# Performance work log

Hardware: AMD Instinct MI355X
Metric: run time of the kernel (lower is better)

The kernel has to match this reference:

```python
import jax, jax.numpy as jnp
import numpy as np

N = 50000
E = 250000
NUM_ETYPES = 4
H = 2  # num_heads
EPS = 1e-12


def _gat_conv(x, W, al, ar, b, src, dst):
    # x: (N, in_dim); W: (in_dim, H*D); al/ar/b: (H, D); src/dst: (E,)
    D = al.shape[-1]
    feat = (x @ W).reshape(-1, H, D)            # (N, H, D)
    el = jnp.sum(feat * al, axis=-1)            # (N, H)
    er = jnp.sum(feat * ar, axis=-1)            # (N, H)
    e = jax.nn.leaky_relu(el[src] + er[dst], 0.2)   # (E, H)
    emax = jax.ops.segment_max(e, dst, num_segments=N)
    ex = jnp.exp(e - emax[dst])
    denom = jax.ops.segment_sum(ex, dst, num_segments=N)
    alpha = ex / denom[dst]                     # (E, H) segment softmax over in-edges
    msg = feat[src] * alpha[:, :, None]         # (E, H, D)
    out = jax.ops.segment_sum(msg, dst, num_segments=N)  # (N, H, D)
    return out + b


def _hetero_layer(x, W, al, ar, b, edges):
    # vmap GATConv over the edge-type axis, then HeteroGraphConv aggregate='mean'
    outs = jax.vmap(lambda w, a, r, bb, e: _gat_conv(x, w, a, r, bb, e[0], e[1]))(
        W, al, ar, b, edges)                    # (T, N, H, D)
    return jnp.mean(outs, axis=0)               # (N, H, D)


def _post(v):
    # relu -> F.normalize(dim=1, i.e. across heads) -> dropout(eval: identity) -> mean over heads
    v = jax.nn.relu(v)
    norm = jnp.sqrt(jnp.sum(v * v, axis=1, keepdims=True))
    v = v / jnp.maximum(norm, EPS)
    return jnp.mean(v, axis=1)                  # (N, D)


def setup_inputs() -> dict:
    key = jax.random.key(0)
    ks = jax.random.split(key, 16)
    s = 0.05
    inp = {
        'x': jax.random.normal(ks[0], (N, 23), jnp.float32),
        'edges': jax.random.randint(ks[1], (NUM_ETYPES, 2, E), 0, N, jnp.int32),
        'W0': jax.random.normal(ks[2], (NUM_ETYPES, 23, H * 64), jnp.float32) * s,
        'al0': jax.random.normal(ks[3], (NUM_ETYPES, H, 64), jnp.float32) * s,
        'ar0': jax.random.normal(ks[4], (NUM_ETYPES, H, 64), jnp.float32) * s,
        'b0': jnp.zeros((NUM_ETYPES, H, 64), jnp.float32),
        'W1': jax.random.normal(ks[5], (NUM_ETYPES, 64, H * 64), jnp.float32) * s,
        'al1': jax.random.normal(ks[6], (NUM_ETYPES, H, 64), jnp.float32) * s,
        'ar1': jax.random.normal(ks[7], (NUM_ETYPES, H, 64), jnp.float32) * s,
        'b1': jnp.zeros((NUM_ETYPES, H, 64), jnp.float32),
        'W2': jax.random.normal(ks[8], (NUM_ETYPES, 64, H * 64), jnp.float32) * s,
        'al2': jax.random.normal(ks[9], (NUM_ETYPES, H, 64), jnp.float32) * s,
        'ar2': jax.random.normal(ks[10], (NUM_ETYPES, H, 64), jnp.float32) * s,
        'b2': jnp.zeros((NUM_ETYPES, H, 64), jnp.float32),
    }
    return inp


def reference(x, edges, W0, al0, ar0, b0, W1, al1, ar1, b1, W2, al2, ar2, b2):
    h = x  # feature_by_level, feat_level=0
    h = _post(_hetero_layer(h, W0, al0, ar0, b0, edges))
    h = _post(_hetero_layer(h, W1, al1, ar1, b1, edges))
    h = jnp.mean(_hetero_layer(h, W2, al2, ar2, b2, edges), axis=1)  # (N, out_dim)
    out = jnp.mean(h, axis=0, keepdims=True)    # dgl.mean_nodes, single graph -> (1, out_dim)
    return out
```

## Files before the change

kernel.cpp:

```cpp
#include <hip/hip_runtime.h>

#define NN 50000
#define NE 250000
#define SCAN_LEN (4*NN)
#define SCAN_BLKS ((SCAN_LEN + 255)/256)
#define EDGE_BLKS ((4*NE + 255)/256)

typedef __attribute__((ext_vector_type(8))) short bf16x8;
typedef __attribute__((ext_vector_type(4))) float f32x4;

__device__ inline ushort f2bf(float f) {
  uint u = __float_as_uint(f);
  return (ushort)((u + 0x7fffu + ((u >> 16) & 1u)) >> 16);
}
__device__ inline float bf2f(ushort b) { return __uint_as_float(((uint)b) << 16); }

__global__ __launch_bounds__(256) void zero_ints(int* __restrict__ p, int n) {
  int i = blockIdx.x*256 + threadIdx.x;
  if (i < n) p[i] = 0;
}
__global__ __launch_bounds__(256) void zero_floats(float* __restrict__ p, int n) {
  int i = blockIdx.x*256 + threadIdx.x;
  if (i < n) p[i] = 0.f;
}

__global__ __launch_bounds__(256) void count_kernel(const int* __restrict__ edges, int* __restrict__ counts) {
  int idx = blockIdx.x*256 + threadIdx.x;
  if (idx >= 4*NE) return;
  int t = idx / NE, e = idx - t*NE;
  int dst = edges[(size_t)t*2*NE + NE + e];
  atomicAdd(&counts[t*NN + dst], 1);
}

__global__ __launch_bounds__(256) void scan1_kernel(const int* __restrict__ in, int* __restrict__ out, int* __restrict__ bsum) {
  __shared__ int sd[256];
  int i = blockIdx.x*256 + threadIdx.x;
  int v = (i < SCAN_LEN) ? in[i] : 0;
  sd[threadIdx.x] = v;
  __syncthreads();
  for (int off = 1; off < 256; off <<= 1) {
    int add = (threadIdx.x >= off) ? sd[threadIdx.x - off] : 0;
    __syncthreads();
    sd[threadIdx.x] += add;
    __syncthreads();
  }
  if (i < SCAN_LEN) out[i] = sd[threadIdx.x] - v;
  if (threadIdx.x == 255) bsum[blockIdx.x] = sd[255];
}

__global__ __launch_bounds__(1024) void scan2_kernel(int* __restrict__ bsum, int nb) {
  __shared__ int sd[1024];
  int i = threadIdx.x;
  int v = (i < nb) ? bsum[i] : 0;
  sd[i] = v;
  __syncthreads();
  for (int off = 1; off < 1024; off <<= 1) {
    int add = (i >= off) ? sd[i - off] : 0;
    __syncthreads();
    sd[i] += add;
    __syncthreads();
  }
  if (i < nb) bsum[i] = sd[i] - v;
}

__global__ __launch_bounds__(256) void scan3_kernel(int* __restrict__ row_ptr, const int* __restrict__ bsum, int* __restrict__ cursor) {
  int i = blockIdx.x*256 + threadIdx.x;
  if (i < SCAN_LEN) {
    int val = row_ptr[i] + bsum[blockIdx.x];
    row_ptr[i] = val;
    cursor[i] = val;
  }
  if (i == 0) row_ptr[SCAN_LEN] = 4*NE;
}

__global__ __launch_bounds__(256) void scatter_kernel(const int* __restrict__ edges, int* __restrict__ cursor, int* __restrict__ col_idx) {
  int idx = blockIdx.x*256 + threadIdx.x;
  if (idx >= 4*NE) return;
  int t = idx / NE, e = idx - t*NE;
  int src = edges[(size_t)t*2*NE + e];
  int dst = edges[(size_t)t*2*NE + NE + e];
  int pos = atomicAdd(&cursor[t*NN + dst], 1);
  col_idx[pos] = src;
}

__global__ __launch_bounds__(256) void convert_x_kernel(const float* __restrict__ x, ushort* __restrict__ xpad) {
  int i = blockIdx.x*256 + threadIdx.x;
  if (i >= NN*64) return;
  int k = i & 63, n = i >> 6;
  xpad[i] = (k < 23) ? f2bf(x[n*23 + k]) : (ushort)0;
}
__global__ __launch_bounds__(256) void convert_wt_kernel(const float* __restrict__ W, ushort* __restrict__ WTg, int Kin) {
  int i = blockIdx.x*256 + threadIdx.x;
  if (i >= 4*128*64) return;
  int k = i & 63, c = (i >> 6) & 127, t = i >> 13;
  float w = (k < Kin) ? W[((size_t)t*Kin + k)*128 + c] : 0.f;
  WTg[i] = f2bf(w);
}

__global__ __launch_bounds__(256)
void gemm_mfma_kernel(const ushort* __restrict__ hbf,
                      const ushort* __restrict__ WTg,
                      const float* __restrict__ alall, const float* __restrict__ arall,
                      ushort* __restrict__ feat, float* __restrict__ el, float* __restrict__ er)
{
  __shared__ ushort WT[128*64];
  const int t = blockIdx.y;
  const int tid = threadIdx.x;
  const int wv = tid >> 6, lane = tid & 63;
  const int node0 = blockIdx.x*64;

  {
    const ushort* src = WTg + (size_t)t*128*64;
    #pragma unroll
    for (int q = 0; q < 4; ++q) {
      int cc = tid + q*256;
      int c = cc >> 3, jj = cc & 7;
      bf16x8 val = *(const bf16x8*)(src + cc*8);
      *(bf16x8*)((char*)WT + c*128 + ((jj ^ (c & 7))*16)) = val;
    }
  }
  __syncthreads();

  const int mrow = lane & 15;
  const int kq = lane >> 4;
  const int anode = node0 + wv*16 + mrow;

  const bf16x8 a0 = *(const bf16x8*)(hbf + (size_t)anode*64 + kq*8);
  const bf16x8 a1 = *(const bf16x8*)(hbf + (size_t)anode*64 + 32 + kq*8);

  f32x4 acc[8];
  #pragma unroll
  for (int nb = 0; nb < 8; ++nb) acc[nb] = (f32x4){0.f,0.f,0.f,0.f};

  #pragma unroll
  for (int nb = 0; nb < 8; ++nb) {
    const int c = nb*16 + mrow;
    const bf16x8 b0 = *(const bf16x8*)((const char*)WT + c*128 + ((kq       ^ (c&7))*16));
    const bf16x8 b1 = *(const bf16x8*)((const char*)WT + c*128 + (((4 + kq) ^ (c&7))*16));
    acc[nb] = __builtin_amdgcn_mfma_f32_16x16x32_bf16(a0, b0, acc[nb], 0, 0, 0);
    acc[nb] = __builtin_amdgcn_mfma_f32_16x16x32_bf16(a1, b1, acc[nb], 0, 0, 0);
  }

  float elp[4][2] = {{0,0},{0,0},{0,0},{0,0}};
  float erp[4][2] = {{0,0},{0,0},{0,0},{0,0}};
  const int noder = node0 + wv*16 + kq*4;
  #pragma unroll
  for (int nb = 0; nb < 8; ++nb) {
    const int c = nb*16 + mrow;
    const float alv = alall[t*128 + c];
    const float arv = arall[t*128 + c];
    const int head = nb >> 2;
    #pragma unroll
    for (int r = 0; r < 4; ++r) {
      elp[r][head] += acc[nb][r]*alv;
      erp[r][head] += acc[nb][r]*arv;
      if (noder + r < NN)
        feat[((size_t)t*NN + noder + r)*128 + c] = f2bf(acc[nb][r]);
    }
  }
  #pragma unroll
  for (int off = 1; off < 16; off <<= 1) {
    #pragma unroll
    for (int r = 0; r < 4; ++r) {
      elp[r][0] += __shfl_xor(elp[r][0], off); elp[r][1] += __shfl_xor(elp[r][1], off);
      erp[r][0] += __shfl_xor(erp[r][0], off); erp[r][1] += __shfl_xor(erp[r][1], off);
    }
  }
  if (mrow == 0) {
    #pragma unroll
    for (int r = 0; r < 4; ++r) {
      if (noder + r < NN) {
        const size_t ix = ((size_t)t*NN + noder + r)*2;
        el[ix]   = elp[r][0]; el[ix+1] = elp[r][1];
        er[ix]   = erp[r][0]; er[ix+1] = erp[r][1];
      }
    }
  }
}

__global__ __launch_bounds__(256)
void gat_node_kernel(const ushort* __restrict__ feat, const float* __restrict__ el,
                     const float* __restrict__ er, const int* __restrict__ row_ptr,
                     const int* __restrict__ col_idx, const float* __restrict__ ball,
                     ushort* __restrict__ hout, int post)
{
  const int v = __builtin_amdgcn_readfirstlane(blockIdx.x*4 + (threadIdx.x >> 6));
  const int lane = threadIdx.x & 63;
  const int half = lane >> 5;
  const int j = lane & 31;

  float ax = 0.f, ay = 0.f;

  for (int t = 0; t < 4; ++t) {
    const int rp0 = row_ptr[t*NN + v];
    const int deg = row_ptr[t*NN + v + 1] - rp0;
    if (deg <= 0) continue;
    const float* elt = el + (size_t)t*NN*2;
    const uint* ftu = (const uint*)(feat + (size_t)t*NN*128);
    const float2 epair = *(const float2*)&er[((size_t)t*NN + v)*2];
    const float erv = half ? epair.y : epair.x;

    float s_run = 0.f, tx = 0.f, ty = 0.f;
    for (int base = 0; base < deg; base += 32) {
      const int cnt = min(32, deg - base);
      int s = 0; float p = 0.f;
      if (j < cnt) {
        s = col_idx[rp0 + base + j];
        float u = elt[s*2 + half] + erv;
        u = (u > 0.f) ? u : 0.2f*u;
        p = __expf(fminf(fmaxf(u, -60.f), 60.f));
      }
      float ps = p;
      #pragma unroll
      for (int off = 16; off; off >>= 1) ps += __shfl_xor(ps, off);
      s_run += ps;

      const uint pbits = __float_as_uint(p);
      const int cnt4 = (cnt + 3) & ~3;
      for (int q0 = 0; q0 < cnt4; q0 += 4) {
        #pragma unroll
        for (int u4 = 0; u4 < 4; ++u4) {
          const int q = q0 + u4;
          const int   sq  = __builtin_amdgcn_readlane(s, q);
          const float pq0 = __uint_as_float(__builtin_amdgcn_readlane(pbits, q));
          const float pq1 = __uint_as_float(__builtin_amdgcn_readlane(pbits, 32 + q));
          const float pq  = half ? pq1 : pq0;
          const uint w = ftu[(uint)sq*64u + (uint)lane];
          tx += pq * __uint_as_float(w << 16);
          ty += pq * __uint_as_float(w & 0xffff0000u);
        }
      }
    }
    const float inv = 1.f / s_run;
    ax += tx*inv; ay += ty*inv;
  }

  const int d0 = lane*2;
  float bx = 0.f, by = 0.f;
  #pragma unroll
  for (int t = 0; t < 4; ++t) { bx += ball[t*128 + d0]; by += ball[t*128 + d0 + 1]; }
  ax = 0.25f*(ax + bx); ay = 0.25f*(ay + by);

  if (post) { ax = fmaxf(ax, 0.f); ay = fmaxf(ay, 0.f); }
  const float px = __shfl_xor(ax, 32), py = __shfl_xor(ay, 32);
  if (lane < 32) {
    float ox, oy;
    if (post) {
      ox = 0.5f*(ax + px)/fmaxf(sqrtf(ax*ax + px*px), 1e-12f);
      oy = 0.5f*(ay + py)/fmaxf(sqrtf(ay*ay + py*py), 1e-12f);
    } else {
      ox = 0.5f*(ax + px); oy = 0.5f*(ay + py);
    }
    const uint pk = (uint)f2bf(ox) | ((uint)f2bf(oy) << 16);
    *(uint*)(hout + (size_t)v*64 + d0) = pk;
  }
}

__global__ __launch_bounds__(256) void reduce_nodes(const ushort* __restrict__ hn, float* __restrict__ accum) {
  __shared__ float sd[256];
  int d = threadIdx.x & 63, rg = threadIdx.x >> 6;
  float s = 0.f;
  for (int r = blockIdx.x*4 + rg; r < NN; r += gridDim.x*4) s += bf2f(hn[(size_t)r*64 + d]);
  sd[threadIdx.x] = s;
  __syncthreads();
  if (threadIdx.x < 64) {
    s = sd[threadIdx.x] + sd[threadIdx.x+64] + sd[threadIdx.x+128] + sd[threadIdx.x+192];
    atomicAdd(&accum[threadIdx.x], s);
  }
}
__global__ __launch_bounds__(64) void final_out_kernel(const float* __restrict__ accum, float* __restrict__ out) {
  int d = threadIdx.x;
  if (d < 64) out[d] = accum[d] * (1.0f/NN);
}

extern "C" void kernel_launch(void* const* d_in, const int* in_sizes, int n_in,
                              void* d_out, int out_size, void* d_ws, size_t ws_size,
                              hipStream_t stream) {
  const float* x     = (const float*)d_in[0];
  const int*   edges = (const int*)d_in[1];
  const float* W[3]  = {(const float*)d_in[2], (const float*)d_in[6], (const float*)d_in[10]};
  const float* al[3] = {(const float*)d_in[3], (const float*)d_in[7], (const float*)d_in[11]};
  const float* ar[3] = {(const float*)d_in[4], (const float*)d_in[8], (const float*)d_in[12]};
  const float* b[3]  = {(const float*)d_in[5], (const float*)d_in[9], (const float*)d_in[13]};

  char* ws = (char*)d_ws;
  auto up = [](size_t x_) { return (x_ + 255) & ~(size_t)255; };

  const size_t szFeat = (size_t)4*NN*128*sizeof(ushort);
  const size_t szEl   = (size_t)4*NN*2*sizeof(float);
  const size_t szHB   = (size_t)(NN+64)*64*sizeof(ushort);
  const size_t szWT   = (size_t)4*128*64*sizeof(ushort);
  const size_t szRp   = (size_t)(4*NN+1)*sizeof(int);
  const size_t szCnt  = (size_t)4*NN*sizeof(int);
  const size_t szCi   = (size_t)4*NE*sizeof(int);

  size_t o = 0;
  ushort* feat  = (ushort*)(ws + o); o += up(szFeat);
  float* elbuf  = (float*)(ws + o);  o += up(szEl);
  float* erbuf  = (float*)(ws + o);  o += up(szEl);
  ushort* xpad  = (ushort*)(ws + o); o += up(szHB);
  ushort* hbuf  = (ushort*)(ws + o); o += up(szHB);
  ushort* WTg   = (ushort*)(ws + o); o += up(szWT);
  float* accum  = (float*)(ws + o);  o += up(256);
  int* row_ptr  = (int*)(ws + o);    o += up(szRp);
  int* cursor   = (int*)(ws + o);    o += up(szCnt);
  int* counts   = (int*)(ws + o);    o += up(szCnt);
  int* col_idx  = (int*)(ws + o);    o += up(szCi);
  int* bsum     = (int*)(ws + o);    o += up(4096);

  zero_ints<<<(4*NN + 255)/256, 256, 0, stream>>>(counts, 4*NN);
  count_kernel<<<EDGE_BLKS, 256, 0, stream>>>(edges, counts);
  scan1_kernel<<<SCAN_BLKS, 256, 0, stream>>>(counts, row_ptr, bsum);
  scan2_kernel<<<1, 1024, 0, stream>>>(bsum, SCAN_BLKS);
  scan3_kernel<<<SCAN_BLKS, 256, 0, stream>>>(row_ptr, bsum, cursor);
  scatter_kernel<<<EDGE_BLKS, 256, 0, stream>>>(edges, cursor, col_idx);

  convert_x_kernel<<<(NN*64 + 255)/256, 256, 0, stream>>>(x, xpad);

  const int gemmGX = (NN + 63)/64;

  for (int l = 0; l < 3; ++l) {
    const ushort* hin = (l == 0) ? xpad : hbuf;
    convert_wt_kernel<<<(4*128*64 + 255)/256, 256, 0, stream>>>(W[l], WTg, (l == 0) ? 23 : 64);
    gemm_mfma_kernel<<<dim3(gemmGX, 4), 256, 0, stream>>>(hin, WTg, al[l], ar[l], feat, elbuf, erbuf);
    gat_node_kernel<<<NN/4, 256, 0, stream>>>(feat, elbuf, erbuf, row_ptr, col_idx, b[l], hbuf, (l < 2) ? 1 : 0);
  }

  zero_floats<<<1, 64, 0, stream>>>(accum, 64);
  reduce_nodes<<<256, 256, 0, stream>>>(hbuf, accum);
  final_out_kernel<<<1, 64, 0, stream>>>(accum, (float*)d_out);
}
```

Baseline: 410.5 us.

## Merge per-type CSR into per-node CSR, precompute edge softmax weights, fold attention into GEMM

Builds one CSR keyed by destination node, with per-type sub-ranges and source indices offset by type, so the gather kernel walks all four edge types for a node in one contiguous range. Attention logits el/er are folded into the GEMM as four extra weight columns (W·a precomputed). A separate edge-parallel kernel computes the exp weights, and the gather kernel becomes a simple per-edge loop without readlane broadcasts. Features are stored with head-interleaved packing so each lane handles one dimension for both heads. The cost is an extra edge pass per layer plus posmap/pexp buffers. Logits are now rounded to bf16 through the MFMA path, which lowers precision.

```diff
diff --git a/kernel.cpp b/kernel.cpp
--- a/kernel.cpp
+++ b/kernel.cpp
@@ -2,8 +2,7 @@
 
 #define NN 50000
 #define NE 250000
-#define SCAN_LEN (4*NN)
-#define SCAN_BLKS ((SCAN_LEN + 255)/256)
+#define NSCAN_BLKS ((NN + 255)/256)
 #define EDGE_BLKS ((4*NE + 255)/256)
 
 typedef __attribute__((ext_vector_type(8))) short bf16x8;
@@ -32,10 +31,15 @@
   atomicAdd(&counts[t*NN + dst], 1);
 }
 
-__global__ __launch_bounds__(256) void scan1_kernel(const int* __restrict__ in, int* __restrict__ out, int* __restrict__ bsum) {
+__global__ __launch_bounds__(256) void sumdeg_kernel(const int* __restrict__ counts, int* __restrict__ totdeg) {
+  int v = blockIdx.x*256 + threadIdx.x;
+  if (v < NN) totdeg[v] = counts[v] + counts[NN+v] + counts[2*NN+v] + counts[3*NN+v];
+}
+
+__global__ __launch_bounds__(256) void scan1_kernel(const int* __restrict__ in, int* __restrict__ out, int* __restrict__ bsum, int n) {
   __shared__ int sd[256];
   int i = blockIdx.x*256 + threadIdx.x;
-  int v = (i < SCAN_LEN) ? in[i] : 0;
+  int v = (i < n) ? in[i] : 0;
   sd[threadIdx.x] = v;
   __syncthreads();
   for (int off = 1; off < 256; off <<= 1) {
@@ -44,7 +48,7 @@
     sd[threadIdx.x] += add;
     __syncthreads();
   }
-  if (i < SCAN_LEN) out[i] = sd[threadIdx.x] - v;
+  if (i < n) out[i] = sd[threadIdx.x] - v;
   if (threadIdx.x == 255) bsum[blockIdx.x] = sd[255];
 }
 
@@ -63,24 +67,34 @@
   if (i < nb) bsum[i] = sd[i] - v;
 }
 
-__global__ __launch_bounds__(256) void scan3_kernel(int* __restrict__ row_ptr, const int* __restrict__ bsum, int* __restrict__ cursor) {
-  int i = blockIdx.x*256 + threadIdx.x;
-  if (i < SCAN_LEN) {
-    int val = row_ptr[i] + bsum[blockIdx.x];
-    row_ptr[i] = val;
-    cursor[i] = val;
-  }
-  if (i == 0) row_ptr[SCAN_LEN] = 4*NE;
-}
-
-__global__ __launch_bounds__(256) void scatter_kernel(const int* __restrict__ edges, int* __restrict__ cursor, int* __restrict__ col_idx) {
+__global__ __launch_bounds__(256) void scan3b_kernel(int* __restrict__ rp, const int* __restrict__ bsum, int n, int total) {
+  int i = blockIdx.x*256 + threadIdx.x;
+  if (i < n) rp[i] += bsum[blockIdx.x];
+  if (i == 0) rp[n] = total;
+}
+
+__global__ __launch_bounds__(256) void make_cursor_kernel(const int* __restrict__ rp2, const int* __restrict__ counts,
+                                                          int* __restrict__ cursor, int* __restrict__ sub_ptr) {
+  int v = blockIdx.x*256 + threadIdx.x;
+  if (v >= NN) return;
+  int b = rp2[v];
+  int s1 = b  + counts[v];
+  int s2 = s1 + counts[NN+v];
+  int s3 = s2 + counts[2*NN+v];
+  cursor[v] = b; cursor[NN+v] = s1; cursor[2*NN+v] = s2; cursor[3*NN+v] = s3;
+  sub_ptr[NN+v] = s1; sub_ptr[2*NN+v] = s2; sub_ptr[3*NN+v] = s3;
+}
+
+__global__ __launch_bounds__(256) void scatter2_kernel(const int* __restrict__ edges, int* __restrict__ cursor,
+                                                       int* __restrict__ col2, int* __restrict__ posmap) {
   int idx = blockIdx.x*256 + threadIdx.x;
   if (idx >= 4*NE) return;
   int t = idx / NE, e = idx - t*NE;
   int src = edges[(size_t)t*2*NE + e];
   int dst = edges[(size_t)t*2*NE + NE + e];
   int pos = atomicAdd(&cursor[t*NN + dst], 1);
-  col_idx[pos] = src;
+  col2[pos] = t*NN + src;
+  posmap[idx] = pos;
 }
 
 __global__ __launch_bounds__(256) void convert_x_kernel(const float* __restrict__ x, ushort* __restrict__ xpad) {
@@ -89,33 +103,43 @@
   int k = i & 63, n = i >> 6;
   xpad[i] = (k < 23) ? f2bf(x[n*23 + k]) : (ushort)0;
 }
-__global__ __launch_bounds__(256) void convert_wt_kernel(const float* __restrict__ W, ushort* __restrict__ WTg, int Kin) {
-  int i = blockIdx.x*256 + threadIdx.x;
-  if (i >= 4*128*64) return;
-  int k = i & 63, c = (i >> 6) & 127, t = i >> 13;
-  float w = (k < Kin) ? W[((size_t)t*Kin + k)*128 + c] : 0.f;
-  WTg[i] = f2bf(w);
+
+__global__ __launch_bounds__(256) void convert_wt2_kernel(const float* __restrict__ W, const float* __restrict__ al,
+                                                          const float* __restrict__ ar, ushort* __restrict__ WTg2, int Kin) {
+  int i = blockIdx.x*256 + threadIdx.x;
+  if (i >= 4*144*64) return;
+  int k = i & 63; int c = (i >> 6) % 144; int t = i / (144*64);
+  float val = 0.f;
+  if (c < 128) {
+    val = (k < Kin) ? W[((size_t)t*Kin + k)*128 + c] : 0.f;
+  } else if (c < 132 && k < Kin) {
+    int m = c - 128, h = m & 1;
+    const float* A = ((m < 2) ? al : ar) + t*128 + h*64;
+    const float* wrow = W + ((size_t)t*Kin + k)*128 + h*64;
+    float s = 0.f;
+    for (int c2 = 0; c2 < 64; ++c2) s += wrow[c2]*A[c2];
+    val = s;
+  }
+  WTg2[((size_t)t*144 + c)*64 + k] = f2bf(val);
 }
 
 __global__ __launch_bounds__(256)
 void gemm_mfma_kernel(const ushort* __restrict__ hbf,
-                      const ushort* __restrict__ WTg,
-                      const float* __restrict__ alall, const float* __restrict__ arall,
-                      ushort* __restrict__ feat, float* __restrict__ el, float* __restrict__ er)
+                      const ushort* __restrict__ WTg2,
+                      uint* __restrict__ featu,
+                      float* __restrict__ elr)
 {
-  __shared__ ushort WT[128*64];
+  __shared__ ushort WT[144*64];
   const int t = blockIdx.y;
   const int tid = threadIdx.x;
   const int wv = tid >> 6, lane = tid & 63;
   const int node0 = blockIdx.x*64;
 
   {
-    const ushort* src = WTg + (size_t)t*128*64;
-    #pragma unroll
-    for (int q = 0; q < 4; ++q) {
-      int cc = tid + q*256;
-      int c = cc >> 3, jj = cc & 7;
-      bf16x8 val = *(const bf16x8*)(src + cc*8);
+    const ushort* src = WTg2 + (size_t)t*144*64;
+    for (int i = tid; i < 1152; i += 256) {
+      int c = i >> 3, jj = i & 7;
+      bf16x8 val = *(const bf16x8*)(src + (size_t)c*64 + jj*8);
       *(bf16x8*)((char*)WT + c*128 + ((jj ^ (c & 7))*16)) = val;
     }
   }
@@ -128,12 +152,12 @@
   const bf16x8 a0 = *(const bf16x8*)(hbf + (size_t)anode*64 + kq*8);
   const bf16x8 a1 = *(const bf16x8*)(hbf + (size_t)anode*64 + 32 + kq*8);
 
-  f32x4 acc[8];
-  #pragma unroll
-  for (int nb = 0; nb < 8; ++nb) acc[nb] = (f32x4){0.f,0.f,0.f,0.f};
-
-  #pragma unroll
-  for (int nb = 0; nb < 8; ++nb) {
+  f32x4 acc[9];
+  #pragma unroll
+  for (int nb = 0; nb < 9; ++nb) acc[nb] = (f32x4){0.f,0.f,0.f,0.f};
+
+  #pragma unroll
+  for (int nb = 0; nb < 9; ++nb) {
     const int c = nb*16 + mrow;
     const bf16x8 b0 = *(const bf16x8*)((const char*)WT + c*128 + ((kq       ^ (c&7))*16));
     const bf16x8 b1 = *(const bf16x8*)((const char*)WT + c*128 + (((4 + kq) ^ (c&7))*16));
@@ -141,119 +165,93 @@
     acc[nb] = __builtin_amdgcn_mfma_f32_16x16x32_bf16(a1, b1, acc[nb], 0, 0, 0);
   }
 
-  float elp[4][2] = {{0,0},{0,0},{0,0},{0,0}};
-  float erp[4][2] = {{0,0},{0,0},{0,0},{0,0}};
   const int noder = node0 + wv*16 + kq*4;
   #pragma unroll
-  for (int nb = 0; nb < 8; ++nb) {
-    const int c = nb*16 + mrow;
-    const float alv = alall[t*128 + c];
-    const float arv = arall[t*128 + c];
-    const int head = nb >> 2;
-    #pragma unroll
-    for (int r = 0; r < 4; ++r) {
-      elp[r][head] += acc[nb][r]*alv;
-      erp[r][head] += acc[nb][r]*arv;
-      if (noder + r < NN)
-        feat[((size_t)t*NN + noder + r)*128 + c] = f2bf(acc[nb][r]);
-    }
-  }
-  #pragma unroll
-  for (int off = 1; off < 16; off <<= 1) {
-    #pragma unroll
-    for (int r = 0; r < 4; ++r) {
-      elp[r][0] += __shfl_xor(elp[r][0], off); elp[r][1] += __shfl_xor(elp[r][1], off);
-      erp[r][0] += __shfl_xor(erp[r][0], off); erp[r][1] += __shfl_xor(erp[r][1], off);
-    }
-  }
-  if (mrow == 0) {
+  for (int nb = 0; nb < 4; ++nb) {
+    const int d = nb*16 + mrow;
     #pragma unroll
     for (int r = 0; r < 4; ++r) {
       if (noder + r < NN) {
-        const size_t ix = ((size_t)t*NN + noder + r)*2;
-        el[ix]   = elp[r][0]; el[ix+1] = elp[r][1];
-        er[ix]   = erp[r][0]; er[ix+1] = erp[r][1];
+        const uint pk = (uint)f2bf(acc[nb][r]) | ((uint)f2bf(acc[nb+4][r]) << 16);
+        featu[((size_t)t*NN + noder + r)*64 + d] = pk;
       }
     }
   }
+  if (mrow < 4) {
+    #pragma unroll
+    for (int r = 0; r < 4; ++r) {
+      if (noder + r < NN)
+        elr[(size_t)(mrow*4 + t)*NN + noder + r] = acc[8][r];
+    }
+  }
 }
 
 __global__ __launch_bounds__(256)
-void gat_node_kernel(const ushort* __restrict__ feat, const float* __restrict__ el,
-                     const float* __restrict__ er, const int* __restrict__ row_ptr,
-                     const int* __restrict__ col_idx, const float* __restrict__ ball,
-                     ushort* __restrict__ hout, int post)
+void phaseA_kernel(const int* __restrict__ edges, const float* __restrict__ elr,
+                   const int* __restrict__ posmap, float* __restrict__ pexp)
+{
+  int idx = blockIdx.x*256 + threadIdx.x;
+  if (idx >= 4*NE) return;
+  int t = idx / NE, e = idx - t*NE;
+  int src = edges[(size_t)t*2*NE + e];
+  int dst = edges[(size_t)t*2*NE + NE + e];
+  float u0 = elr[(size_t)(0*4+t)*NN + src] + elr[(size_t)(2*4+t)*NN + dst];
+  float u1 = elr[(size_t)(1*4+t)*NN + src] + elr[(size_t)(3*4+t)*NN + dst];
+  u0 = (u0 > 0.f) ? u0 : 0.2f*u0;
+  u1 = (u1 > 0.f) ? u1 : 0.2f*u1;
+  float p0 = __expf(fminf(fmaxf(u0, -60.f), 60.f));
+  float p1 = __expf(fminf(fmaxf(u1, -60.f), 60.f));
+  int pos = posmap[idx];
+  ((float2*)pexp)[pos] = make_float2(p0, p1);
+}
+
+__global__ __launch_bounds__(256)
+void gather_kernel(const uint* __restrict__ featu, const float* __restrict__ pexp,
+                   const int* __restrict__ col2, const int* __restrict__ row_ptr2,
+                   const int* __restrict__ sub_ptr, const float* __restrict__ ball,
+                   ushort* __restrict__ hout, int post)
 {
   const int v = __builtin_amdgcn_readfirstlane(blockIdx.x*4 + (threadIdx.x >> 6));
   const int lane = threadIdx.x & 63;
-  const int half = lane >> 5;
-  const int j = lane & 31;
+
+  const int b0 = row_ptr2[v];
+  const int b4 = row_ptr2[v+1];
+  const int s1 = sub_ptr[NN+v], s2 = sub_ptr[2*NN+v], s3 = sub_ptr[3*NN+v];
+  const int bounds[5] = {b0, s1, s2, s3, b4};
 
   float ax = 0.f, ay = 0.f;
 
+  #pragma unroll
   for (int t = 0; t < 4; ++t) {
-    const int rp0 = row_ptr[t*NN + v];
-    const int deg = row_ptr[t*NN + v + 1] - rp0;
-    if (deg <= 0) continue;
-    const float* elt = el + (size_t)t*NN*2;
-    const uint* ftu = (const uint*)(feat + (size_t)t*NN*128);
-    const float2 epair = *(const float2*)&er[((size_t)t*NN + v)*2];
-    const float erv = half ? epair.y : epair.x;
-
-    float s_run = 0.f, tx = 0.f, ty = 0.f;
-    for (int base = 0; base < deg; base += 32) {
-      const int cnt = min(32, deg - base);
-      int s = 0; float p = 0.f;
-      if (j < cnt) {
-        s = col_idx[rp0 + base + j];
-        float u = elt[s*2 + half] + erv;
-        u = (u > 0.f) ? u : 0.2f*u;
-        p = __expf(fminf(fmaxf(u, -60.f), 60.f));
-      }
-      float ps = p;
-      #pragma unroll
-      for (int off = 16; off; off >>= 1) ps += __shfl_xor(ps, off);
-      s_run += ps;
-
-      const uint pbits = __float_as_uint(p);
-      const int cnt4 = (cnt + 3) & ~3;
-      for (int q0 = 0; q0 < cnt4; q0 += 4) {
-        #pragma unroll
-        for (int u4 = 0; u4 < 4; ++u4) {
-          const int q = q0 + u4;
-          const int   sq  = __builtin_amdgcn_readlane(s, q);
-          const float pq0 = __uint_as_float(__builtin_amdgcn_readlane(pbits, q));
-          const float pq1 = __uint_as_float(__builtin_amdgcn_readlane(pbits, 32 + q));
-          const float pq  = half ? pq1 : pq0;
-          const uint w = ftu[(uint)sq*64u + (uint)lane];
-          tx += pq * __uint_as_float(w << 16);
-          ty += pq * __uint_as_float(w & 0xffff0000u);
-        }
-      }
+    const int lo = bounds[t], hi = bounds[t+1];
+    if (lo >= hi) continue;
+    float sum0 = 0.f, sum1 = 0.f, tx = 0.f, ty = 0.f;
+    #pragma unroll 4
+    for (int q = lo; q < hi; ++q) {
+      const int c = col2[q];
+      const float2 p = ((const float2*)pexp)[q];
+      sum0 += p.x; sum1 += p.y;
+      const uint w = featu[(uint)c*64u + (uint)lane];
+      tx += p.x * __uint_as_float(w << 16);
+      ty += p.y * __uint_as_float(w & 0xffff0000u);
     }
-    const float inv = 1.f / s_run;
-    ax += tx*inv; ay += ty*inv;
-  }
-
-  const int d0 = lane*2;
+    ax += tx * __builtin_amdgcn_rcpf(sum0);
+    ay += ty * __builtin_amdgcn_rcpf(sum1);
+  }
+
   float bx = 0.f, by = 0.f;
   #pragma unroll
-  for (int t = 0; t < 4; ++t) { bx += ball[t*128 + d0]; by += ball[t*128 + d0 + 1]; }
+  for (int t = 0; t < 4; ++t) { bx += ball[t*128 + lane]; by += ball[t*128 + 64 + lane]; }
   ax = 0.25f*(ax + bx); ay = 0.25f*(ay + by);
 
-  if (post) { ax = fmaxf(ax, 0.f); ay = fmaxf(ay, 0.f); }
-  const float px = __shfl_xor(ax, 32), py = __shfl_xor(ay, 32);
-  if (lane < 32) {
-    float ox, oy;
-    if (post) {
-      ox = 0.5f*(ax + px)/fmaxf(sqrtf(ax*ax + px*px), 1e-12f);
-      oy = 0.5f*(ay + py)/fmaxf(sqrtf(ay*ay + py*py), 1e-12f);
-    } else {
-      ox = 0.5f*(ax + px); oy = 0.5f*(ay + py);
-    }
-    const uint pk = (uint)f2bf(ox) | ((uint)f2bf(oy) << 16);
-    *(uint*)(hout + (size_t)v*64 + d0) = pk;
-  }
+  float o;
+  if (post) {
+    ax = fmaxf(ax, 0.f); ay = fmaxf(ay, 0.f);
+    o = 0.5f*(ax + ay) / fmaxf(sqrtf(ax*ax + ay*ay), 1e-12f);
+  } else {
+    o = 0.5f*(ax + ay);
+  }
+  hout[(size_t)v*64 + lane] = f2bf(o);
 }
 
 __global__ __launch_bounds__(256) void reduce_nodes(const ushort* __restrict__ hn, float* __restrict__ accum) {
@@ -286,34 +284,40 @@
   char* ws = (char*)d_ws;
   auto up = [](size_t x_) { return (x_ + 255) & ~(size_t)255; };
 
-  const size_t szFeat = (size_t)4*NN*128*sizeof(ushort);
-  const size_t szEl   = (size_t)4*NN*2*sizeof(float);
+  const size_t szFeat = (size_t)4*NN*64*sizeof(uint);
+  const size_t szElr  = (size_t)16*NN*sizeof(float);
+  const size_t szPex  = (size_t)4*NE*2*sizeof(float);
+  const size_t szPM   = (size_t)4*NE*sizeof(int);
   const size_t szHB   = (size_t)(NN+64)*64*sizeof(ushort);
-  const size_t szWT   = (size_t)4*128*64*sizeof(ushort);
-  const size_t szRp   = (size_t)(4*NN+1)*sizeof(int);
-  const size_t szCnt  = (size_t)4*NN*sizeof(int);
-  const size_t szCi   = (size_t)4*NE*sizeof(int);
+  const size_t szWT   = (size_t)4*144*64*sizeof(ushort);
+  const size_t szI4   = (size_t)4*NN*sizeof(int);
+  const size_t szI1   = (size_t)(NN+1)*sizeof(int);
 
   size_t o = 0;
-  ushort* feat  = (ushort*)(ws + o); o += up(szFeat);
-  float* elbuf  = (float*)(ws + o);  o += up(szEl);
-  float* erbuf  = (float*)(ws + o);  o += up(szEl);
-  ushort* xpad  = (ushort*)(ws + o); o += up(szHB);
-  ushort* hbuf  = (ushort*)(ws + o); o += up(szHB);
-  ushort* WTg   = (ushort*)(ws + o); o += up(szWT);
-  float* accum  = (float*)(ws + o);  o += up(256);
-  int* row_ptr  = (int*)(ws + o);    o += up(szRp);
-  int* cursor   = (int*)(ws + o);    o += up(szCnt);
-  int* counts   = (int*)(ws + o);    o += up(szCnt);
-  int* col_idx  = (int*)(ws + o);    o += up(szCi);
-  int* bsum     = (int*)(ws + o);    o += up(4096);
+  uint*   featu  = (uint*)(ws + o);   o += up(szFeat);
+  float*  elr    = (float*)(ws + o);  o += up(szElr);
+  float*  pexp   = (float*)(ws + o);  o += up(szPex);
+  int*    posmap = (int*)(ws + o);    o += up(szPM);
+  int*    col2   = (int*)(ws + o);    o += up(szPM);
+  ushort* xpad   = (ushort*)(ws + o); o += up(szHB);
+  ushort* hbuf   = (ushort*)(ws + o); o += up(szHB);
+  ushort* WTg2   = (ushort*)(ws + o); o += up(szWT);
+  float*  accum  = (float*)(ws + o);  o += up(256);
+  int* row_ptr2  = (int*)(ws + o);    o += up(szI1);
+  int* totdeg    = (int*)(ws + o);    o += up(szI1);
+  int* cursor    = (int*)(ws + o);    o += up(szI4);
+  int* counts    = (int*)(ws + o);    o += up(szI4);
+  int* sub_ptr   = (int*)(ws + o);    o += up(szI4);
+  int* bsum      = (int*)(ws + o);    o += up(4096);
 
   zero_ints<<<(4*NN + 255)/256, 256, 0, stream>>>(counts, 4*NN);
   count_kernel<<<EDGE_BLKS, 256, 0, stream>>>(edges, counts);
-  scan1_kernel<<<SCAN_BLKS, 256, 0, stream>>>(counts, row_ptr, bsum);
-  scan2_kernel<<<1, 1024, 0, stream>>>(bsum, SCAN_BLKS);
-  scan3_kernel<<<SCAN_BLKS, 256, 0, stream>>>(row_ptr, bsum, cursor);
-  scatter_kernel<<<EDGE_BLKS, 256, 0, stream>>>(edges, cursor, col_idx);
+  sumdeg_kernel<<<NSCAN_BLKS, 256, 0, stream>>>(counts, totdeg);
+  scan1_kernel<<<NSCAN_BLKS, 256, 0, stream>>>(totdeg, row_ptr2, bsum, NN);
+  scan2_kernel<<<1, 1024, 0, stream>>>(bsum, NSCAN_BLKS);
+  scan3b_kernel<<<NSCAN_BLKS, 256, 0, stream>>>(row_ptr2, bsum, NN, 4*NE);
+  make_cursor_kernel<<<NSCAN_BLKS, 256, 0, stream>>>(row_ptr2, counts, cursor, sub_ptr);
+  scatter2_kernel<<<EDGE_BLKS, 256, 0, stream>>>(edges, cursor, col2, posmap);
 
   convert_x_kernel<<<(NN*64 + 255)/256, 256, 0, stream>>>(x, xpad);
 
@@ -321,9 +325,10 @@
 
   for (int l = 0; l < 3; ++l) {
     const ushort* hin = (l == 0) ? xpad : hbuf;
-    convert_wt_kernel<<<(4*128*64 + 255)/256, 256, 0, stream>>>(W[l], WTg, (l == 0) ? 23 : 64);
-    gemm_mfma_kernel<<<dim3(gemmGX, 4), 256, 0, stream>>>(hin, WTg, al[l], ar[l], feat, elbuf, erbuf);
-    gat_node_kernel<<<NN/4, 256, 0, stream>>>(feat, elbuf, erbuf, row_ptr, col_idx, b[l], hbuf, (l < 2) ? 1 : 0);
+    convert_wt2_kernel<<<(4*144*64 + 255)/256, 256, 0, stream>>>(W[l], al[l], ar[l], WTg2, (l == 0) ? 23 : 64);
+    gemm_mfma_kernel<<<dim3(gemmGX, 4), 256, 0, stream>>>(hin, WTg2, featu, elr);
+    phaseA_kernel<<<EDGE_BLKS, 256, 0, stream>>>(edges, elr, posmap, pexp);
+    gather_kernel<<<NN/4, 256, 0, stream>>>(featu, pexp, col2, row_ptr2, sub_ptr, b[l], hbuf, (l < 2) ? 1 : 0);
   }
 
   zero_floats<<<1, 64, 0, stream>>>(accum, 64);
```

Result: slower. 428.4 us (+4.4%).
